# Kernel tuning notes

Measured on AMD Instinct MI355X. Metric: run time of the kernel, lower is better.

## Reference

```python
import jax, jax.numpy as jnp
import numpy as np
import math

IN_C = 1024
OUT_C = 1024
HEADS = 16
GROUPS = 4

def grouped_linear(src, weight, bias):
    # src: [..., in_c]; weight: [g, in_c//g, out_c//g]; bias: [out_c]
    g, icg, ocg = weight.shape
    lead = src.shape[:-1]
    s = src.reshape(*lead, g, icg)
    out = jnp.einsum('...gi,gio->...go', s, weight)
    out = out.reshape(*lead, g * ocg)
    return out + bias

def restricted_softmax(src, margin=0.0):
    src_max = jnp.maximum(jnp.max(src, axis=-1, keepdims=True), 0.0)
    out = jnp.exp(src - src_max)
    return out / (jnp.sum(out, axis=-1, keepdims=True) + jnp.exp(margin - src_max))

def setup_inputs() -> dict:
    key = jax.random.key(0)
    ks = jax.random.split(key, 9)
    B, S = 2, 2048
    icg, ocg = IN_C // GROUPS, OUT_C // GROUPS
    scale = 1.0 / math.sqrt(icg)
    return {
        'query': jax.random.normal(ks[0], (B, S, IN_C), jnp.float32),
        'key': jax.random.normal(ks[1], (B, S, IN_C), jnp.float32),
        'value': jax.random.normal(ks[2], (B, S, IN_C), jnp.float32),
        'wq': jax.random.uniform(ks[3], (GROUPS, icg, ocg), jnp.float32, -scale, scale),
        'wk': jax.random.uniform(ks[4], (GROUPS, icg, ocg), jnp.float32, -scale, scale),
        'wv': jax.random.uniform(ks[5], (GROUPS, icg, ocg), jnp.float32, -scale, scale),
        'bq': jax.random.uniform(ks[6], (OUT_C,), jnp.float32, -scale, scale),
        'bk': jax.random.uniform(ks[7], (OUT_C,), jnp.float32, -scale, scale),
        'bv': jax.random.uniform(ks[8], (OUT_C,), jnp.float32, -scale, scale),
    }

def reference(query, key, value, wq, wk, wv, bq, bk, bv):
    q = grouped_linear(query, wq, bq)   # [B,S,OUT_C]
    k = grouped_linear(key, wk, bk)
    v = grouped_linear(value, wv, bv)
    B, Sq, _ = q.shape
    Sk = k.shape[-2]
    d = OUT_C // HEADS
    q = q.reshape(B, Sq, HEADS, d).transpose(0, 2, 1, 3)  # [B,H,Sq,d]
    k = k.reshape(B, Sk, HEADS, d).transpose(0, 2, 1, 3)
    v = v.reshape(B, Sk, HEADS, d).transpose(0, 2, 1, 3)
    score = jnp.einsum('bhqd,bhkd->bhqk', q, k) / math.sqrt(d)
    attn = restricted_softmax(score)
    out = jnp.einsum('bhqk,bhkd->bhqd', attn, v)
    out = out.transpose(0, 2, 1, 3).reshape(B, Sq, OUT_C)
    return out
```

## Files before the change

kernel.cpp:

```cpp
#include <hip/hip_runtime.h>
#include <hip/hip_bf16.h>

#define BB 2
#define SS 2048
#define CC 1024
#define HH 16
#define DDIM 64
#define NROWS (BB*SS)

#define QSC 0.18033688011112042f

typedef __attribute__((ext_vector_type(8))) short bf16x8;
typedef __attribute__((ext_vector_type(4))) float f32x4;

__device__ __forceinline__ f32x4 mfma16(bf16x8 a, bf16x8 b, f32x4 c) {
    return __builtin_amdgcn_mfma_f32_16x16x32_bf16(a, b, c, 0, 0, 0);
}

__global__ __launch_bounds__(256) void prep_wt(
    const float* __restrict__ wq, const float* __restrict__ wk,
    const float* __restrict__ wv, __hip_bfloat16* __restrict__ wt)
{
    const float* w = blockIdx.z == 0 ? wq : blockIdx.z == 1 ? wk : wv;
    const int g  = blockIdx.y;
    const int kt = blockIdx.x >> 2;
    const int nt = blockIdx.x & 3;
    __shared__ __hip_bfloat16 Ls[64][72];
    const int t = threadIdx.x;
    #pragma unroll
    for (int j = 0; j < 4; ++j) {
        int f4 = t + j*256;
        int row = f4 >> 4, n0 = (f4 & 15) * 4;
        float4 f = *(const float4*)&w[(size_t)g*65536 + (size_t)(kt*64+row)*256
                                      + nt*64 + n0];
        Ls[n0+0][row] = __float2bfloat16(f.x);
        Ls[n0+1][row] = __float2bfloat16(f.y);
        Ls[n0+2][row] = __float2bfloat16(f.z);
        Ls[n0+3][row] = __float2bfloat16(f.w);
    }
    __syncthreads();
    #pragma unroll
    for (int j = 0; j < 2; ++j) {
        int u = t + j*256;
        int nr = u >> 3, k8 = (u & 7) * 8;
        *(uint4*)&wt[((size_t)(blockIdx.z*4 + g)*256 + nt*64 + nr)*256
                     + kt*64 + k8] = *(const uint4*)&Ls[nr][k8];
    }
}

__global__ __launch_bounds__(256, 3) void proj_mfma(
    const float* __restrict__ qin, const float* __restrict__ kin,
    const float* __restrict__ vin,
    const __hip_bfloat16* __restrict__ wt,
    const float* __restrict__ bq, const float* __restrict__ bk,
    const float* __restrict__ bv,
    __hip_bfloat16* __restrict__ qs, __hip_bfloat16* __restrict__ ks_,
    __hip_bfloat16* __restrict__ vs)
{
    const int z = blockIdx.z;
    const float* src; const float* bias;
    if (z == 0)      { src = qin; bias = bq; }
    else if (z == 1) { src = kin; bias = bk; }
    else             { src = vin; bias = bv; }

    const int hp   = blockIdx.y;
    const int g    = hp >> 1;
    const int col0 = (hp & 1) * 128;
    const int row0 = blockIdx.x * 128;
    const int b    = row0 >> 11;
    const int s0   = row0 & 2047;

    __shared__ char smem[36864];
    auto As = (__hip_bfloat16 (*)[72])smem;
    auto Ws = (__hip_bfloat16 (*)[72])(smem + 18432);

    const int t    = threadIdx.x;
    const int wid  = t >> 6;
    const int lane = t & 63;
    const int l16  = lane & 15;
    const int quad = lane >> 4;

    f32x4 acc[2][8];
    #pragma unroll
    for (int mt = 0; mt < 2; ++mt)
        #pragma unroll
        for (int nt = 0; nt < 8; ++nt) acc[mt][nt] = (f32x4){0.f,0.f,0.f,0.f};

    const __hip_bfloat16* wtz = wt + (size_t)(z*4 + g)*65536;

    for (int kt = 0; kt < 4; ++kt) {
        __syncthreads();
        #pragma unroll
        for (int j = 0; j < 8; ++j) {
            int idx = t + j*256;
            int row = idx >> 4, c4 = (idx & 15) * 4;
            float4 f = *(const float4*)&src[(size_t)(row0 + row)*CC + g*256
                                            + kt*64 + c4];
            union { __hip_bfloat16 hh[4]; uint2 u; } pk;
            pk.hh[0] = __float2bfloat16(f.x); pk.hh[1] = __float2bfloat16(f.y);
            pk.hh[2] = __float2bfloat16(f.z); pk.hh[3] = __float2bfloat16(f.w);
            *(uint2*)&As[row][c4] = pk.u;
        }
        #pragma unroll
        for (int j = 0; j < 4; ++j) {
            int idx = t + j*256;
            int n = idx >> 3, k8 = (idx & 7) * 8;
            *(uint4*)&Ws[n][k8] =
                *(const uint4*)&wtz[(size_t)(col0 + n)*256 + kt*64 + k8];
        }
        __syncthreads();
        #pragma unroll
        for (int kss = 0; kss < 2; ++kss) {
            bf16x8 af[2], wf[8];
            #pragma unroll
            for (int mt = 0; mt < 2; ++mt)
                af[mt] = *(const bf16x8*)&As[wid*32 + mt*16 + l16][kss*32 + quad*8];
            #pragma unroll
            for (int nt = 0; nt < 8; ++nt)
                wf[nt] = *(const bf16x8*)&Ws[nt*16 + l16][kss*32 + quad*8];
            #pragma unroll
            for (int mt = 0; mt < 2; ++mt)
                #pragma unroll
                for (int nt = 0; nt < 8; ++nt)
                    acc[mt][nt] = mfma16(af[mt], wf[nt], acc[mt][nt]);
        }
    }

    float bval[8];
    #pragma unroll
    for (int nt = 0; nt < 8; ++nt) bval[nt] = bias[g*256 + col0 + nt*16 + l16];

    __syncthreads();

    if (z < 2) {
        const float scale = (z == 0) ? QSC : 1.0f;
        auto Ot = (__hip_bfloat16 (*)[136])smem;
        #pragma unroll
        for (int mt = 0; mt < 2; ++mt)
            #pragma unroll
            for (int nt = 0; nt < 8; ++nt)
                #pragma unroll
                for (int r = 0; r < 4; ++r)
                    Ot[wid*32 + mt*16 + quad*4 + r][nt*16 + l16] =
                        __float2bfloat16((acc[mt][nt][r] + bval[nt]) * scale);
        __syncthreads();
        __hip_bfloat16* base = (z == 0) ? qs : ks_;
        #pragma unroll
        for (int j = 0; j < 8; ++j) {
            int f = wid + j*4;
            int hl = f >> 4, t16l = (f >> 1) & 7, kcs = f & 1;
            uint4 v = *(const uint4*)&Ot[t16l*16 + l16][hl*64 + kcs*32 + quad*8];
            int h = hp*2 + hl;
            int t16g = (s0 >> 4) + t16l;
            *(uint4*)&base[((size_t)(b*HH + h) << 17)
                           + ((size_t)(t16g*2 + kcs) << 9) + lane*8] = v;
        }
    } else {
        auto Vl = (__hip_bfloat16 (*)[136])smem;
        #pragma unroll
        for (int mt = 0; mt < 2; ++mt)
            #pragma unroll
            for (int nt = 0; nt < 8; ++nt) {
                union { __hip_bfloat16 hh[4]; uint2 u; } pk;
                #pragma unroll
                for (int r = 0; r < 4; ++r)
                    pk.hh[r] = __float2bfloat16(acc[mt][nt][r] + bval[nt]);
                *(uint2*)&Vl[nt*16 + l16][wid*32 + mt*16 + quad*4] = pk.u;
            }
        __syncthreads();
        const int kc0 = s0 >> 5;
        #pragma unroll
        for (int j = 0; j < 8; ++j) {
            int f = wid + j*4;
            int hl = f >> 4, dt = (f >> 2) & 3, kcl = f & 3;
            uint4 v = *(const uint4*)&Vl[hl*64 + dt*16 + l16][kcl*32 + quad*8];
            int h = hp*2 + hl;
            *(uint4*)&vs[((size_t)(b*HH + h) << 17)
                         + ((size_t)(dt*64 + kc0 + kcl) << 9) + lane*8] = v;
        }
    }
}

__global__ __launch_bounds__(256, 2) void attn_mfma(
    const __hip_bfloat16* __restrict__ qs, const __hip_bfloat16* __restrict__ ks_,
    const __hip_bfloat16* __restrict__ vs, float* __restrict__ out)
{
    const int qt = blockIdx.x;
    const int h  = blockIdx.y;
    const int b  = blockIdx.z;

    __shared__ __hip_bfloat16 Ps[4][64][72];
    __shared__ float Uls[2][64][68];
    __shared__ float Lls[2][64];

    const int t    = threadIdx.x;
    const int wid  = t >> 6;
    const int qsub = wid & 1;
    const int kh   = wid >> 1;
    const int lane = t & 63;
    const int l16  = lane & 15;
    const int quad = lane >> 4;

    const __hip_bfloat16* qb = qs + ((size_t)(b*HH + h) << 17);
    const __hip_bfloat16* kb = ks_ + ((size_t)(b*HH + h) << 17);
    const __hip_bfloat16* vb = vs + ((size_t)(b*HH + h) << 17);

    const bf16x8 onesv = (bf16x8){16256,16256,16256,16256,
                                  16256,16256,16256,16256};

    bf16x8 qf[4][2];
    #pragma unroll
    for (int mt = 0; mt < 4; ++mt)
        #pragma unroll
        for (int kss = 0; kss < 2; ++kss)
            qf[mt][kss] = *(const bf16x8*)(qb +
                ((size_t)((qt*8 + qsub*4 + mt)*2 + kss) << 9) + lane*8);

    f32x4 O[4][4];
    f32x4 Lfrag[4];
    #pragma unroll
    for (int mt = 0; mt < 4; ++mt) {
        Lfrag[mt] = (f32x4){0.f,0.f,0.f,0.f};
        #pragma unroll
        for (int dt = 0; dt < 4; ++dt) O[mt][dt] = (f32x4){0.f,0.f,0.f,0.f};
    }

    bf16x8 kf[4][2];
    #pragma unroll
    for (int nt = 0; nt < 4; ++nt)
        #pragma unroll
        for (int kss = 0; kss < 2; ++kss)
            kf[nt][kss] = *(const bf16x8*)(kb +
                ((size_t)((kh*64 + nt)*2 + kss) << 9) + lane*8);

    for (int kt = 0; kt < 16; ++kt) {
        bf16x8 vf[4][2];
        #pragma unroll
        for (int dt = 0; dt < 4; ++dt)
            #pragma unroll
            for (int kss = 0; kss < 2; ++kss)
                vf[dt][kss] = *(const bf16x8*)(vb +
                    ((size_t)(dt*64 + kh*32 + kt*2 + kss) << 9) + lane*8);

        #pragma unroll
        for (int nt = 0; nt < 4; ++nt) {
            f32x4 st[4];
            #pragma unroll
            for (int mt = 0; mt < 4; ++mt) {
                f32x4 z = (f32x4){0.f,0.f,0.f,0.f};
                z = mfma16(kf[nt][0], qf[mt][0], z);
                st[mt] = mfma16(kf[nt][1], qf[mt][1], z);
            }
            #pragma unroll
            for (int mt = 0; mt < 4; ++mt) {
                float2 e0, e1;
                e0.x = __builtin_amdgcn_exp2f(st[mt][0]);
                e0.y = __builtin_amdgcn_exp2f(st[mt][1]);
                e1.x = __builtin_amdgcn_exp2f(st[mt][2]);
                e1.y = __builtin_amdgcn_exp2f(st[mt][3]);
                union { __hip_bfloat162 h2[2]; uint2 u; } pk;
                pk.h2[0] = __float22bfloat162_rn(e0);
                pk.h2[1] = __float22bfloat162_rn(e1);
                *(uint2*)&Ps[wid][mt*16 + l16][nt*16 + quad*4] = pk.u;
            }
        }

        if (kt + 1 < 16) {
            #pragma unroll
            for (int nt = 0; nt < 4; ++nt)
                #pragma unroll
                for (int kss = 0; kss < 2; ++kss)
                    kf[nt][kss] = *(const bf16x8*)(kb +
                        ((size_t)((kh*64 + (kt+1)*4 + nt)*2 + kss) << 9) + lane*8);
        }

        #pragma unroll
        for (int kss = 0; kss < 2; ++kss) {
            bf16x8 pf[4];
            #pragma unroll
            for (int mt = 0; mt < 4; ++mt)
                pf[mt] = *(const bf16x8*)&Ps[wid][mt*16 + l16][kss*32 + quad*8];
            #pragma unroll
            for (int mt = 0; mt < 4; ++mt) {
                Lfrag[mt] = mfma16(onesv, pf[mt], Lfrag[mt]);
                #pragma unroll
                for (int dt = 0; dt < 4; ++dt)
                    O[mt][dt] = mfma16(vf[dt][kss], pf[mt], O[mt][dt]);
            }
        }
    }

    if (kh == 1) {
        #pragma unroll
        for (int mt = 0; mt < 4; ++mt) {
            if (quad == 0) Lls[qsub][mt*16 + l16] = Lfrag[mt][0];
            #pragma unroll
            for (int dt = 0; dt < 4; ++dt) {
                float4 u4;
                u4.x = O[mt][dt][0]; u4.y = O[mt][dt][1];
                u4.z = O[mt][dt][2]; u4.w = O[mt][dt][3];
                *(float4*)&Uls[qsub][mt*16 + l16][dt*16 + quad*4] = u4;
            }
        }
    }
    __syncthreads();
    if (kh == 0) {
        #pragma unroll
        for (int mt = 0; mt < 4; ++mt) {
            const float inv = 1.0f /
                (1.0f + Lfrag[mt][0] + Lls[qsub][mt*16 + l16]);
            const size_t row = (size_t)b*SS + qt*128 + qsub*64 + mt*16 + l16;
            #pragma unroll
            for (int dt = 0; dt < 4; ++dt) {
                float4 u4 = *(const float4*)&Uls[qsub][mt*16 + l16][dt*16 + quad*4];
                float4 o4;
                o4.x = (O[mt][dt][0] + u4.x) * inv;
                o4.y = (O[mt][dt][1] + u4.y) * inv;
                o4.z = (O[mt][dt][2] + u4.z) * inv;
                o4.w = (O[mt][dt][3] + u4.w) * inv;
                *(float4*)&out[row*CC + h*DDIM + dt*16 + quad*4] = o4;
            }
        }
    }
}

extern "C" void kernel_launch(void* const* d_in, const int* in_sizes, int n_in,
                              void* d_out, int out_size, void* d_ws, size_t ws_size,
                              hipStream_t stream) {
    (void)in_sizes; (void)n_in; (void)out_size; (void)ws_size;
    const float* qin = (const float*)d_in[0];
    const float* kin = (const float*)d_in[1];
    const float* vin = (const float*)d_in[2];
    const float* wq  = (const float*)d_in[3];
    const float* wk  = (const float*)d_in[4];
    const float* wv  = (const float*)d_in[5];
    const float* bq  = (const float*)d_in[6];
    const float* bk  = (const float*)d_in[7];
    const float* bv  = (const float*)d_in[8];

    char* w0 = (char*)d_ws;
    __hip_bfloat16* qs = (__hip_bfloat16*)(w0);
    __hip_bfloat16* ks = (__hip_bfloat16*)(w0 + 8388608);
    __hip_bfloat16* vs = (__hip_bfloat16*)(w0 + 16777216);
    __hip_bfloat16* wt = (__hip_bfloat16*)(w0 + 25165824);
    float* out = (float*)d_out;

    prep_wt<<<dim3(16, 4, 3), 256, 0, stream>>>(wq, wk, wv, wt);
    proj_mfma<<<dim3(32, 8, 3), 256, 0, stream>>>(
        qin, kin, vin, wt, bq, bk, bv, qs, ks, vs);
    attn_mfma<<<dim3(16, 16, 2), 256, 0, stream>>>(qs, ks, vs, out);
}
```

Baseline: 161.9 us.

## Retile projection to full group width and software-pipeline attention P·V stage

The projection kernel now gives each block 64 rows by the full 256-column group, so each input tile is read and converted to bf16 once per group rather than twice. The output is written back in two 128-column passes. The attention loop is software-pipelined: the P·V MFMAs for the previous key tile run after the score/exp work for the current tile, using a double-buffered P array in LDS, so exp and MFMA work can overlap. LDS row paddings change to 76/140 to alter bank mapping, and the reduction buffer now aliases the P buffer, with an extra barrier before it is reused.

```diff
diff --git a/kernel.cpp b/kernel.cpp
--- a/kernel.cpp
+++ b/kernel.cpp
@@ -25,7 +25,7 @@
     const int g  = blockIdx.y;
     const int kt = blockIdx.x >> 2;
     const int nt = blockIdx.x & 3;
-    __shared__ __hip_bfloat16 Ls[64][72];
+    __shared__ __hip_bfloat16 Ls[64][76];
     const int t = threadIdx.x;
     #pragma unroll
     for (int j = 0; j < 4; ++j) {
@@ -63,16 +63,14 @@
     else if (z == 1) { src = kin; bias = bk; }
     else             { src = vin; bias = bv; }
 
-    const int hp   = blockIdx.y;
-    const int g    = hp >> 1;
-    const int col0 = (hp & 1) * 128;
-    const int row0 = blockIdx.x * 128;
+    const int g    = blockIdx.y;
+    const int row0 = blockIdx.x * 64;
     const int b    = row0 >> 11;
     const int s0   = row0 & 2047;
 
-    __shared__ char smem[36864];
-    auto As = (__hip_bfloat16 (*)[72])smem;
-    auto Ws = (__hip_bfloat16 (*)[72])(smem + 18432);
+    __shared__ char smem[48640];
+    auto As = (__hip_bfloat16 (*)[76])smem;
+    auto Ws = (__hip_bfloat16 (*)[76])(smem + 9728);
 
     const int t    = threadIdx.x;
     const int wid  = t >> 6;
@@ -80,18 +78,16 @@
     const int l16  = lane & 15;
     const int quad = lane >> 4;
 
-    f32x4 acc[2][8];
-    #pragma unroll
-    for (int mt = 0; mt < 2; ++mt)
-        #pragma unroll
-        for (int nt = 0; nt < 8; ++nt) acc[mt][nt] = (f32x4){0.f,0.f,0.f,0.f};
+    f32x4 acc[16];
+    #pragma unroll
+    for (int nt = 0; nt < 16; ++nt) acc[nt] = (f32x4){0.f,0.f,0.f,0.f};
 
     const __hip_bfloat16* wtz = wt + (size_t)(z*4 + g)*65536;
 
     for (int kt = 0; kt < 4; ++kt) {
         __syncthreads();
         #pragma unroll
-        for (int j = 0; j < 8; ++j) {
+        for (int j = 0; j < 4; ++j) {
             int idx = t + j*256;
             int row = idx >> 4, c4 = (idx & 15) * 4;
             float4 f = *(const float4*)&src[(size_t)(row0 + row)*CC + g*256
@@ -102,81 +98,77 @@
             *(uint2*)&As[row][c4] = pk.u;
         }
         #pragma unroll
-        for (int j = 0; j < 4; ++j) {
+        for (int j = 0; j < 8; ++j) {
             int idx = t + j*256;
             int n = idx >> 3, k8 = (idx & 7) * 8;
             *(uint4*)&Ws[n][k8] =
-                *(const uint4*)&wtz[(size_t)(col0 + n)*256 + kt*64 + k8];
+                *(const uint4*)&wtz[(size_t)n*256 + kt*64 + k8];
         }
         __syncthreads();
         #pragma unroll
         for (int kss = 0; kss < 2; ++kss) {
-            bf16x8 af[2], wf[8];
-            #pragma unroll
-            for (int mt = 0; mt < 2; ++mt)
-                af[mt] = *(const bf16x8*)&As[wid*32 + mt*16 + l16][kss*32 + quad*8];
-            #pragma unroll
-            for (int nt = 0; nt < 8; ++nt)
-                wf[nt] = *(const bf16x8*)&Ws[nt*16 + l16][kss*32 + quad*8];
-            #pragma unroll
-            for (int mt = 0; mt < 2; ++mt)
-                #pragma unroll
-                for (int nt = 0; nt < 8; ++nt)
-                    acc[mt][nt] = mfma16(af[mt], wf[nt], acc[mt][nt]);
-        }
-    }
-
-    float bval[8];
-    #pragma unroll
-    for (int nt = 0; nt < 8; ++nt) bval[nt] = bias[g*256 + col0 + nt*16 + l16];
-
-    __syncthreads();
-
-    if (z < 2) {
-        const float scale = (z == 0) ? QSC : 1.0f;
-        auto Ot = (__hip_bfloat16 (*)[136])smem;
-        #pragma unroll
-        for (int mt = 0; mt < 2; ++mt)
-            #pragma unroll
-            for (int nt = 0; nt < 8; ++nt)
+            bf16x8 af = *(const bf16x8*)&As[wid*16 + l16][kss*32 + quad*8];
+            #pragma unroll
+            for (int nt = 0; nt < 16; ++nt) {
+                bf16x8 wf = *(const bf16x8*)&Ws[nt*16 + l16][kss*32 + quad*8];
+                acc[nt] = mfma16(af, wf, acc[nt]);
+            }
+        }
+    }
+
+    float bval[16];
+    #pragma unroll
+    for (int nt = 0; nt < 16; ++nt) bval[nt] = bias[g*256 + nt*16 + l16];
+
+    #pragma unroll
+    for (int p = 0; p < 2; ++p) {
+        __syncthreads();
+        if (z < 2) {
+            const float scale = (z == 0) ? QSC : 1.0f;
+            auto Ot = (__hip_bfloat16 (*)[140])smem;
+            #pragma unroll
+            for (int nt8 = 0; nt8 < 8; ++nt8)
                 #pragma unroll
                 for (int r = 0; r < 4; ++r)
-                    Ot[wid*32 + mt*16 + quad*4 + r][nt*16 + l16] =
-                        __float2bfloat16((acc[mt][nt][r] + bval[nt]) * scale);
-        __syncthreads();
-        __hip_bfloat16* base = (z == 0) ? qs : ks_;
-        #pragma unroll
-        for (int j = 0; j < 8; ++j) {
-            int f = wid + j*4;
-            int hl = f >> 4, t16l = (f >> 1) & 7, kcs = f & 1;
-            uint4 v = *(const uint4*)&Ot[t16l*16 + l16][hl*64 + kcs*32 + quad*8];
-            int h = hp*2 + hl;
-            int t16g = (s0 >> 4) + t16l;
-            *(uint4*)&base[((size_t)(b*HH + h) << 17)
-                           + ((size_t)(t16g*2 + kcs) << 9) + lane*8] = v;
-        }
-    } else {
-        auto Vl = (__hip_bfloat16 (*)[136])smem;
-        #pragma unroll
-        for (int mt = 0; mt < 2; ++mt)
-            #pragma unroll
-            for (int nt = 0; nt < 8; ++nt) {
+                    Ot[wid*16 + quad*4 + r][nt8*16 + l16] =
+                        __float2bfloat16((acc[p*8 + nt8][r] + bval[p*8 + nt8])
+                                         * scale);
+            __syncthreads();
+            __hip_bfloat16* base = (z == 0) ? qs : ks_;
+            #pragma unroll
+            for (int j = 0; j < 4; ++j) {
+                int f = wid + j*4;
+                int hl = f >> 3, t16l = (f >> 1) & 3, kcs = f & 1;
+                uint4 v = *(const uint4*)&Ot[t16l*16 + l16]
+                                            [hl*64 + kcs*32 + quad*8];
+                int h = g*4 + p*2 + hl;
+                int t16g = (s0 >> 4) + t16l;
+                *(uint4*)&base[((size_t)(b*HH + h) << 17)
+                               + ((size_t)(t16g*2 + kcs) << 9) + lane*8] = v;
+            }
+        } else {
+            auto Vl = (__hip_bfloat16 (*)[140])smem;
+            #pragma unroll
+            for (int nt8 = 0; nt8 < 8; ++nt8) {
                 union { __hip_bfloat16 hh[4]; uint2 u; } pk;
                 #pragma unroll
                 for (int r = 0; r < 4; ++r)
-                    pk.hh[r] = __float2bfloat16(acc[mt][nt][r] + bval[nt]);
-                *(uint2*)&Vl[nt*16 + l16][wid*32 + mt*16 + quad*4] = pk.u;
-            }
-        __syncthreads();
-        const int kc0 = s0 >> 5;
-        #pragma unroll
-        for (int j = 0; j < 8; ++j) {
-            int f = wid + j*4;
-            int hl = f >> 4, dt = (f >> 2) & 3, kcl = f & 3;
-            uint4 v = *(const uint4*)&Vl[hl*64 + dt*16 + l16][kcl*32 + quad*8];
-            int h = hp*2 + hl;
-            *(uint4*)&vs[((size_t)(b*HH + h) << 17)
-                         + ((size_t)(dt*64 + kc0 + kcl) << 9) + lane*8] = v;
+                    pk.hh[r] = __float2bfloat16(acc[p*8 + nt8][r]
+                                                + bval[p*8 + nt8]);
+                *(uint2*)&Vl[nt8*16 + l16][wid*16 + quad*4] = pk.u;
+            }
+            __syncthreads();
+            const int kc0 = s0 >> 5;
+            #pragma unroll
+            for (int j = 0; j < 4; ++j) {
+                int f = wid + j*4;
+                int hl = f >> 3, dt = (f >> 1) & 3, kcl = f & 1;
+                uint4 v = *(const uint4*)&Vl[hl*64 + dt*16 + l16]
+                                            [kcl*32 + quad*8];
+                int h = g*4 + p*2 + hl;
+                *(uint4*)&vs[((size_t)(b*HH + h) << 17)
+                             + ((size_t)(dt*64 + kc0 + kcl) << 9) + lane*8] = v;
+            }
         }
     }
 }
@@ -189,9 +181,9 @@
     const int h  = blockIdx.y;
     const int b  = blockIdx.z;
 
-    __shared__ __hip_bfloat16 Ps[4][64][72];
-    __shared__ float Uls[2][64][68];
+    __shared__ __hip_bfloat16 Ps[2][4][64][76];
     __shared__ float Lls[2][64];
+    auto Uls = (float (*)[64][70])&Ps[0][0][0][0];
 
     const int t    = threadIdx.x;
     const int wid  = t >> 6;
@@ -233,63 +225,74 @@
             kf[nt][kss] = *(const bf16x8*)(kb +
                 ((size_t)((kh*64 + nt)*2 + kss) << 9) + lane*8);
 
-    for (int kt = 0; kt < 16; ++kt) {
-        bf16x8 vf[4][2];
-        #pragma unroll
-        for (int dt = 0; dt < 4; ++dt)
-            #pragma unroll
-            for (int kss = 0; kss < 2; ++kss)
-                vf[dt][kss] = *(const bf16x8*)(vb +
-                    ((size_t)(dt*64 + kh*32 + kt*2 + kss) << 9) + lane*8);
-
-        #pragma unroll
-        for (int nt = 0; nt < 4; ++nt) {
-            f32x4 st[4];
-            #pragma unroll
-            for (int mt = 0; mt < 4; ++mt) {
-                f32x4 z = (f32x4){0.f,0.f,0.f,0.f};
-                z = mfma16(kf[nt][0], qf[mt][0], z);
-                st[mt] = mfma16(kf[nt][1], qf[mt][1], z);
-            }
-            #pragma unroll
-            for (int mt = 0; mt < 4; ++mt) {
-                float2 e0, e1;
-                e0.x = __builtin_amdgcn_exp2f(st[mt][0]);
-                e0.y = __builtin_amdgcn_exp2f(st[mt][1]);
-                e1.x = __builtin_amdgcn_exp2f(st[mt][2]);
-                e1.y = __builtin_amdgcn_exp2f(st[mt][3]);
-                union { __hip_bfloat162 h2[2]; uint2 u; } pk;
-                pk.h2[0] = __float22bfloat162_rn(e0);
-                pk.h2[1] = __float22bfloat162_rn(e1);
-                *(uint2*)&Ps[wid][mt*16 + l16][nt*16 + quad*4] = pk.u;
-            }
-        }
-
-        if (kt + 1 < 16) {
-            #pragma unroll
-            for (int nt = 0; nt < 4; ++nt)
+    for (int kt = 0; kt <= 16; ++kt) {
+        const int cur = kt & 1;
+        const int prv = cur ^ 1;
+
+        bf16x8 vfp[4][2];
+        if (kt >= 1) {
+            #pragma unroll
+            for (int dt = 0; dt < 4; ++dt)
                 #pragma unroll
                 for (int kss = 0; kss < 2; ++kss)
-                    kf[nt][kss] = *(const bf16x8*)(kb +
-                        ((size_t)((kh*64 + (kt+1)*4 + nt)*2 + kss) << 9) + lane*8);
-        }
-
-        #pragma unroll
-        for (int kss = 0; kss < 2; ++kss) {
-            bf16x8 pf[4];
-            #pragma unroll
-            for (int mt = 0; mt < 4; ++mt)
-                pf[mt] = *(const bf16x8*)&Ps[wid][mt*16 + l16][kss*32 + quad*8];
-            #pragma unroll
-            for (int mt = 0; mt < 4; ++mt) {
-                Lfrag[mt] = mfma16(onesv, pf[mt], Lfrag[mt]);
-                #pragma unroll
-                for (int dt = 0; dt < 4; ++dt)
-                    O[mt][dt] = mfma16(vf[dt][kss], pf[mt], O[mt][dt]);
-            }
-        }
-    }
-
+                    vfp[dt][kss] = *(const bf16x8*)(vb +
+                        ((size_t)(dt*64 + kh*32 + (kt-1)*2 + kss) << 9) + lane*8);
+        }
+
+        if (kt < 16) {
+            #pragma unroll
+            for (int nt = 0; nt < 4; ++nt) {
+                f32x4 st[4];
+                #pragma unroll
+                for (int mt = 0; mt < 4; ++mt) {
+                    f32x4 z = (f32x4){0.f,0.f,0.f,0.f};
+                    z = mfma16(kf[nt][0], qf[mt][0], z);
+                    st[mt] = mfma16(kf[nt][1], qf[mt][1], z);
+                }
+                #pragma unroll
+                for (int mt = 0; mt < 4; ++mt) {
+                    float2 e0, e1;
+                    e0.x = __builtin_amdgcn_exp2f(st[mt][0]);
+                    e0.y = __builtin_amdgcn_exp2f(st[mt][1]);
+                    e1.x = __builtin_amdgcn_exp2f(st[mt][2]);
+                    e1.y = __builtin_amdgcn_exp2f(st[mt][3]);
+                    union { __hip_bfloat162 h2[2]; uint2 u; } pk;
+                    pk.h2[0] = __float22bfloat162_rn(e0);
+                    pk.h2[1] = __float22bfloat162_rn(e1);
+                    *(uint2*)&Ps[cur][wid][mt*16 + l16][nt*16 + quad*4] = pk.u;
+                }
+            }
+            if (kt + 1 < 16) {
+                #pragma unroll
+                for (int nt = 0; nt < 4; ++nt)
+                    #pragma unroll
+                    for (int kss = 0; kss < 2; ++kss)
+                        kf[nt][kss] = *(const bf16x8*)(kb +
+                            ((size_t)((kh*64 + (kt+1)*4 + nt)*2 + kss) << 9)
+                            + lane*8);
+            }
+        }
+
+        if (kt >= 1) {
+            #pragma unroll
+            for (int kss = 0; kss < 2; ++kss) {
+                bf16x8 pf[4];
+                #pragma unroll
+                for (int mt = 0; mt < 4; ++mt)
+                    pf[mt] = *(const bf16x8*)
+                        &Ps[prv][wid][mt*16 + l16][kss*32 + quad*8];
+                #pragma unroll
+                for (int mt = 0; mt < 4; ++mt) {
+                    Lfrag[mt] = mfma16(onesv, pf[mt], Lfrag[mt]);
+                    #pragma unroll
+                    for (int dt = 0; dt < 4; ++dt)
+                        O[mt][dt] = mfma16(vfp[dt][kss], pf[mt], O[mt][dt]);
+                }
+            }
+        }
+    }
+
+    __syncthreads();
     if (kh == 1) {
         #pragma unroll
         for (int mt = 0; mt < 4; ++mt) {
@@ -312,7 +315,8 @@
             const size_t row = (size_t)b*SS + qt*128 + qsub*64 + mt*16 + l16;
             #pragma unroll
             for (int dt = 0; dt < 4; ++dt) {
-                float4 u4 = *(const float4*)&Uls[qsub][mt*16 + l16][dt*16 + quad*4];
+                float4 u4 = *(const float4*)
+                    &Uls[qsub][mt*16 + l16][dt*16 + quad*4];
                 float4 o4;
                 o4.x = (O[mt][dt][0] + u4.x) * inv;
                 o4.y = (O[mt][dt][1] + u4.y) * inv;
@@ -346,7 +350,7 @@
     float* out = (float*)d_out;
 
     prep_wt<<<dim3(16, 4, 3), 256, 0, stream>>>(wq, wk, wv, wt);
-    proj_mfma<<<dim3(32, 8, 3), 256, 0, stream>>>(
+    proj_mfma<<<dim3(64, 4, 3), 256, 0, stream>>>(
         qin, kin, vin, wt, bq, bk, bv, qs, ks, vs);
     attn_mfma<<<dim3(16, 16, 2), 256, 0, stream>>>(qs, ks, vs, out);
 }
```

Result: slower. 193.9 us (+19.8%).

## Software-pipeline attention loop with double-buffered P tiles in LDS

Applied to the files above, without the earlier changes.

Restructures the attention key loop into a skewed software pipeline. Each iteration computes QK^T, exp2 and the P tile for block kt into one LDS buffer while running the PV MFMAs for block kt-1 from the other buffer, so the dependent exp/LDS store and the MFMA work can interleave. LDS use is held constant by aliasing the cross-wave reduction buffer onto the doubled P buffer, which needs an extra barrier before the epilogue. The cost is more live registers for the prefetched V fragments and one extra loop iteration, which may put pressure on the 2-blocks-per-CU occupancy target.

```diff
diff --git a/kernel.cpp b/kernel.cpp
--- a/kernel.cpp
+++ b/kernel.cpp
@@ -16,6 +16,7 @@
 __device__ __forceinline__ f32x4 mfma16(bf16x8 a, bf16x8 b, f32x4 c) {
     return __builtin_amdgcn_mfma_f32_16x16x32_bf16(a, b, c, 0, 0, 0);
 }
+
 
 __global__ __launch_bounds__(256) void prep_wt(
     const float* __restrict__ wq, const float* __restrict__ wk,
@@ -189,9 +190,9 @@
     const int h  = blockIdx.y;
     const int b  = blockIdx.z;
 
-    __shared__ __hip_bfloat16 Ps[4][64][72];
-    __shared__ float Uls[2][64][68];
+    __shared__ __hip_bfloat16 Ps[2][4][64][72];
     __shared__ float Lls[2][64];
+    auto Uls = (float (*)[64][68])&Ps[0][0][0][0];
 
     const int t    = threadIdx.x;
     const int wid  = t >> 6;
@@ -233,63 +234,74 @@
             kf[nt][kss] = *(const bf16x8*)(kb +
                 ((size_t)((kh*64 + nt)*2 + kss) << 9) + lane*8);
 
-    for (int kt = 0; kt < 16; ++kt) {
-        bf16x8 vf[4][2];
-        #pragma unroll
-        for (int dt = 0; dt < 4; ++dt)
-            #pragma unroll
-            for (int kss = 0; kss < 2; ++kss)
-                vf[dt][kss] = *(const bf16x8*)(vb +
-                    ((size_t)(dt*64 + kh*32 + kt*2 + kss) << 9) + lane*8);
-
-        #pragma unroll
-        for (int nt = 0; nt < 4; ++nt) {
-            f32x4 st[4];
-            #pragma unroll
-            for (int mt = 0; mt < 4; ++mt) {
-                f32x4 z = (f32x4){0.f,0.f,0.f,0.f};
-                z = mfma16(kf[nt][0], qf[mt][0], z);
-                st[mt] = mfma16(kf[nt][1], qf[mt][1], z);
-            }
-            #pragma unroll
-            for (int mt = 0; mt < 4; ++mt) {
-                float2 e0, e1;
-                e0.x = __builtin_amdgcn_exp2f(st[mt][0]);
-                e0.y = __builtin_amdgcn_exp2f(st[mt][1]);
-                e1.x = __builtin_amdgcn_exp2f(st[mt][2]);
-                e1.y = __builtin_amdgcn_exp2f(st[mt][3]);
-                union { __hip_bfloat162 h2[2]; uint2 u; } pk;
-                pk.h2[0] = __float22bfloat162_rn(e0);
-                pk.h2[1] = __float22bfloat162_rn(e1);
-                *(uint2*)&Ps[wid][mt*16 + l16][nt*16 + quad*4] = pk.u;
-            }
-        }
-
-        if (kt + 1 < 16) {
-            #pragma unroll
-            for (int nt = 0; nt < 4; ++nt)
+    for (int kt = 0; kt <= 16; ++kt) {
+        const int cur = kt & 1;
+        const int prv = cur ^ 1;
+
+        bf16x8 vfp[4][2];
+        if (kt >= 1) {
+            #pragma unroll
+            for (int dt = 0; dt < 4; ++dt)
                 #pragma unroll
                 for (int kss = 0; kss < 2; ++kss)
-                    kf[nt][kss] = *(const bf16x8*)(kb +
-                        ((size_t)((kh*64 + (kt+1)*4 + nt)*2 + kss) << 9) + lane*8);
-        }
-
-        #pragma unroll
-        for (int kss = 0; kss < 2; ++kss) {
-            bf16x8 pf[4];
-            #pragma unroll
-            for (int mt = 0; mt < 4; ++mt)
-                pf[mt] = *(const bf16x8*)&Ps[wid][mt*16 + l16][kss*32 + quad*8];
-            #pragma unroll
-            for (int mt = 0; mt < 4; ++mt) {
-                Lfrag[mt] = mfma16(onesv, pf[mt], Lfrag[mt]);
-                #pragma unroll
-                for (int dt = 0; dt < 4; ++dt)
-                    O[mt][dt] = mfma16(vf[dt][kss], pf[mt], O[mt][dt]);
-            }
-        }
-    }
-
+                    vfp[dt][kss] = *(const bf16x8*)(vb +
+                        ((size_t)(dt*64 + kh*32 + (kt-1)*2 + kss) << 9) + lane*8);
+        }
+
+        if (kt < 16) {
+            #pragma unroll
+            for (int nt = 0; nt < 4; ++nt) {
+                f32x4 st[4];
+                #pragma unroll
+                for (int mt = 0; mt < 4; ++mt) {
+                    f32x4 z = (f32x4){0.f,0.f,0.f,0.f};
+                    z = mfma16(kf[nt][0], qf[mt][0], z);
+                    st[mt] = mfma16(kf[nt][1], qf[mt][1], z);
+                }
+                #pragma unroll
+                for (int mt = 0; mt < 4; ++mt) {
+                    float2 e0, e1;
+                    e0.x = __builtin_amdgcn_exp2f(st[mt][0]);
+                    e0.y = __builtin_amdgcn_exp2f(st[mt][1]);
+                    e1.x = __builtin_amdgcn_exp2f(st[mt][2]);
+                    e1.y = __builtin_amdgcn_exp2f(st[mt][3]);
+                    union { __hip_bfloat162 h2[2]; uint2 u; } pk;
+                    pk.h2[0] = __float22bfloat162_rn(e0);
+                    pk.h2[1] = __float22bfloat162_rn(e1);
+                    *(uint2*)&Ps[cur][wid][mt*16 + l16][nt*16 + quad*4] = pk.u;
+                }
+            }
+            if (kt + 1 < 16) {
+                #pragma unroll
+                for (int nt = 0; nt < 4; ++nt)
+                    #pragma unroll
+                    for (int kss = 0; kss < 2; ++kss)
+                        kf[nt][kss] = *(const bf16x8*)(kb +
+                            ((size_t)((kh*64 + (kt+1)*4 + nt)*2 + kss) << 9)
+                            + lane*8);
+            }
+        }
+
+        if (kt >= 1) {
+            #pragma unroll
+            for (int kss = 0; kss < 2; ++kss) {
+                bf16x8 pf[4];
+                #pragma unroll
+                for (int mt = 0; mt < 4; ++mt)
+                    pf[mt] = *(const bf16x8*)
+                        &Ps[prv][wid][mt*16 + l16][kss*32 + quad*8];
+                #pragma unroll
+                for (int mt = 0; mt < 4; ++mt) {
+                    Lfrag[mt] = mfma16(onesv, pf[mt], Lfrag[mt]);
+                    #pragma unroll
+                    for (int dt = 0; dt < 4; ++dt)
+                        O[mt][dt] = mfma16(vfp[dt][kss], pf[mt], O[mt][dt]);
+                }
+            }
+        }
+    }
+
+    __syncthreads();
     if (kh == 1) {
         #pragma unroll
         for (int mt = 0; mt < 4; ++mt) {
@@ -312,7 +324,8 @@
             const size_t row = (size_t)b*SS + qt*128 + qsub*64 + mt*16 + l16;
             #pragma unroll
             for (int dt = 0; dt < 4; ++dt) {
-                float4 u4 = *(const float4*)&Uls[qsub][mt*16 + l16][dt*16 + quad*4];
+                float4 u4 = *(const float4*)
+                    &Uls[qsub][mt*16 + l16][dt*16 + quad*4];
                 float4 o4;
                 o4.x = (O[mt][dt][0] + u4.x) * inv;
                 o4.y = (O[mt][dt][1] + u4.y) * inv;
```

New measurement: 162.1 us. About the same (+0.1%).
